# Optimization experiments

Hardware: AMD Instinct MI355X
Metric: run time of the kernel (lower is better)

Reference implementation:

```python
import jax, jax.numpy as jnp
import numpy as np


def setup_inputs() -> dict:
    key = jax.random.key(0)
    k1, k2, k3, k4 = jax.random.split(key, 4)
    B, S, D = 8, 2048, 512
    scale = 1.0 / np.sqrt(D)
    return {
        "x": jax.random.normal(k1, (B, S, D), dtype=jnp.float32),
        "WQ": jax.random.normal(k2, (D, D), dtype=jnp.float32) * scale,
        "WK": jax.random.normal(k3, (D, D), dtype=jnp.float32) * scale,
        "WV": jax.random.normal(k4, (D, D), dtype=jnp.float32) * scale,
    }


def reference(x, WQ, WK, WV):
    # x: [B, S, D]; single-head scaled dot-product self-attention
    Q = jnp.einsum("bsd,de->bse", x, WQ)
    K = jnp.einsum("bsd,de->bse", x, WK)
    V = jnp.einsum("bsd,de->bse", x, WV)
    d_k = jnp.asarray(K.shape[-1], dtype=x.dtype)
    scores = jnp.einsum("bqd,bkd->bqk", Q, K) / jnp.sqrt(d_k)  # [B,S,S]
    weights = jax.nn.softmax(scores, axis=-1)
    return jnp.einsum("bqk,bkd->bqd", weights, V)
```

## Files before the change

### kernel.cpp

```cpp
#include <hip/hip_runtime.h>
#include <cstdint>
#include <cstddef>

#define B_ 8
#define S_ 2048
#define D_ 512

typedef float f32x4 __attribute__((ext_vector_type(4)));
typedef __bf16 bf16x8 __attribute__((ext_vector_type(8)));

__device__ __forceinline__ unsigned short f2bf(float f) {
    unsigned u = __builtin_bit_cast(unsigned, f);
    u += 0x7FFFu + ((u >> 16) & 1u);
    return (unsigned short)(u >> 16);
}

__device__ __forceinline__ void gll16(const void* g, void* l) {
    __builtin_amdgcn_global_load_lds(
        (const __attribute__((address_space(1))) unsigned int*)g,
        (__attribute__((address_space(3))) unsigned int*)l, 16, 0, 0);
}

#define VMCNT(n) asm volatile("s_waitcnt vmcnt(%0)" :: "i"(n) : "memory")
#define LGKM0()  asm volatile("s_waitcnt lgkmcnt(0)" ::: "memory")
#define SBAR()   __builtin_amdgcn_s_barrier()
#define SCHED0() __builtin_amdgcn_sched_barrier(0)

template<int AMT, int BNT>
__global__ __launch_bounds__(512, 2) void gemm8(
    const unsigned short* __restrict__ A,
    const unsigned short* __restrict__ B,
    void* __restrict__ Cv,
    unsigned short* __restrict__ Cv2,
    int K, int lda, int ldb, int ldc, int ntn)
{
    constexpr int BM     = 64 * AMT;
    constexpr int BN     = 128 * BNT;
    constexpr int ABYTES = BM * 128;
    constexpr int BBYTES = BN * 128;
    constexpr int AH     = ABYTES / 2;
    constexpr int BH     = BBYTES / 2;
    constexpr int AGL    = AMT / 2;
    constexpr int BGL    = BNT;
    constexpr int BUFB   = ABYTES + BBYTES;
    __shared__ __align__(16) char lds[2 * BUFB];

    const int tq  = blockIdx.x;
    const int tn  = tq % ntn;
    const int tm  = tq / ntn;
    const int m0   = tm * BM;
    const int n0   = tn * BN;
    const int tid  = threadIdx.x;
    const int lane = tid & 63;
    const int w    = tid >> 6;
    const int g2   = w >> 2;
    const int nb   = w & 3;

    const int lrow = lane >> 3;
    const int swz  = ((lane & 7) ^ lrow) << 3;
    const unsigned short* gA[2][AGL];
    const unsigned short* gB[2][BGL];
    #pragma unroll
    for (int h = 0; h < 2; ++h) {
        #pragma unroll
        for (int i = 0; i < AGL; ++i)
            gA[h][i] = A + (size_t)(m0 + h * (BM / 2) + (w * AGL + i) * 8 + lrow) * lda + swz;
        #pragma unroll
        for (int i = 0; i < BGL; ++i)
            gB[h][i] = B + (size_t)(n0 + h * (BN / 2) + (w * BGL + i) * 8 + lrow) * ldb + swz;
    }
    auto stA = [&](int bs, int h, int kof) {
        #pragma unroll
        for (int i = 0; i < AGL; ++i)
            gll16(gA[h][i] + kof, lds + bs * BUFB + h * AH + (w * AGL + i) * 1024);
    };
    auto stB = [&](int bs, int h, int kof) {
        #pragma unroll
        for (int i = 0; i < BGL; ++i)
            gll16(gB[h][i] + kof, lds + bs * BUFB + ABYTES + h * BH + (w * BGL + i) * 1024);
    };

    const int fr = lane & 15;
    const int gq = lane >> 4;
    const int c0 = (gq ^ (fr & 7)) << 4;
    int aoff[AMT], boff[BNT];
    #pragma unroll
    for (int ml = 0; ml < AMT; ++ml)
        aoff[ml] = (g2 * (16 * AMT) + ml * 16 + fr) * 128 + c0;
    #pragma unroll
    for (int nl = 0; nl < BNT; ++nl)
        boff[nl] = (nb * (16 * BNT) + nl * 16 + fr) * 128 + c0;

    bf16x8 af[2 * AMT], bLO[2 * BNT], bHI[2 * BNT];
    f32x4 acc[2 * AMT][2 * BNT] = {};

    auto ldA = [&](const char* Ab, int mh) {
        #pragma unroll
        for (int ml = 0; ml < AMT; ++ml)
            #pragma unroll
            for (int kk = 0; kk < 2; ++kk)
                af[ml * 2 + kk] = *(const bf16x8*)(Ab + mh * AH + (aoff[ml] ^ (kk << 6)));
    };
    auto ldB = [&](const char* Bb, int nh, bf16x8* bf) {
        #pragma unroll
        for (int nl = 0; nl < BNT; ++nl)
            #pragma unroll
            for (int kk = 0; kk < 2; ++kk)
                bf[nl * 2 + kk] = *(const bf16x8*)(Bb + nh * BH + (boff[nl] ^ (kk << 6)));
    };
    auto mma = [&](int mh, int nh, const bf16x8* bf) {
        __builtin_amdgcn_s_setprio(1);
        #pragma unroll
        for (int ml = 0; ml < AMT; ++ml)
            #pragma unroll
            for (int nl = 0; nl < BNT; ++nl)
                #pragma unroll
                for (int kk = 0; kk < 2; ++kk)
                    acc[mh * AMT + ml][nh * BNT + nl] =
                        __builtin_amdgcn_mfma_f32_16x16x32_bf16(
                            af[ml * 2 + kk], bf[nl * 2 + kk],
                            acc[mh * AMT + ml][nh * BNT + nl], 0, 0, 0);
        __builtin_amdgcn_s_setprio(0);
    };

    stA(0, 0, 0);  stB(0, 0, 0);
    stA(0, 1, 0);  stB(0, 1, 0);
    stA(1, 0, 64); stB(1, 0, 64);

    const int NT = K >> 6;
    for (int tt = 0; tt < NT; ++tt) {
        const int bs = tt & 1;
        const char* Ab = lds + bs * BUFB;
        const char* Bb = Ab + ABYTES;
        const bool last = (tt == NT - 1);

        if (!last) stA(bs ^ 1, 1, (tt + 1) << 6);
        if (last) { VMCNT(AGL + BGL); } else { VMCNT(6); }
        SBAR(); SCHED0();
        ldA(Ab, 0); ldB(Bb, 0, bLO);
        mma(0, 0, bLO);

        if (!last) stB(bs ^ 1, 1, (tt + 1) << 6);
        if (last) { VMCNT(0); } else { VMCNT(6); }
        SBAR(); SCHED0();
        ldB(Bb, 1, bHI);
        mma(0, 1, bHI);

        if (tt + 2 < NT) stA(bs, 0, (tt + 2) << 6);
        VMCNT(6);
        SBAR(); SCHED0();
        ldA(Ab, 1);
        mma(1, 0, bLO);

        if (tt + 2 < NT) stB(bs, 0, (tt + 2) << 6);
        VMCNT(6);
        SBAR(); SCHED0();
        mma(1, 1, bHI);
    }

    const int rb4 = gq << 2;
#define AB_(mt) ((((mt) / AMT) * (BM / 2)) + g2 * (16 * AMT) + ((mt) % AMT) * 16)
#define BB_(nt) ((((nt) / BNT) * (BN / 2)) + nb * (16 * BNT) + ((nt) % BNT) * 16)
    if (tn >= 4) {
        #pragma unroll
        for (int mt = 0; mt < 2 * AMT; ++mt) {
            const int s0q = m0 + AB_(mt) + rb4;
            const int b   = s0q >> 11;
            const int se  = s0q & (S_ - 1);
            #pragma unroll
            for (int nt = 0; nt < 2 * BNT; ++nt) {
                const int d = (n0 - 2 * D_) + BB_(nt) + fr;
                ushort4 u;
                u.x = f2bf(acc[mt][nt][0]);
                u.y = f2bf(acc[mt][nt][1]);
                u.z = f2bf(acc[mt][nt][2]);
                u.w = f2bf(acc[mt][nt][3]);
                *(ushort4*)&Cv2[((size_t)b * D_ + d) * S_ + se] = u;
            }
        }
    } else {
        unsigned short* C = (unsigned short*)Cv;
        #pragma unroll
        for (int mt = 0; mt < 2 * AMT; ++mt)
            #pragma unroll
            for (int nt = 0; nt < 2 * BNT; ++nt) {
                const int gc = n0 + BB_(nt) + fr;
                #pragma unroll
                for (int r = 0; r < 4; ++r)
                    C[(size_t)(m0 + AB_(mt) + rb4 + r) * ldc + gc] = f2bf(acc[mt][nt][r]);
            }
    }
#undef AB_
#undef BB_
}

__global__ __launch_bounds__(512, 2) void fused_attn(
    const unsigned short* __restrict__ qk,
    const unsigned short* __restrict__ vtb,
    float* __restrict__ out,
    float scale)
{
    __shared__ __align__(16) char lds[148480];
    char* const RING = lds;
    char* const PB   = lds + 131072;
    float* const RS  = (float*)(lds + 147456);

    const int lin = blockIdx.x;
    const int bz  = lin & 7;
    const int q0  = (lin >> 3) * 64;
    const int tid = threadIdx.x;
    const int lane = tid & 63;
    const int w   = tid >> 6;
    const int fr  = lane & 15;
    const int gq  = lane >> 4;
    const int g2  = w >> 2;
    const int nb  = w & 3;
    const int k7  = fr & 7;

    int row4[4], sc4[4];
    #pragma unroll
    for (int i = 0; i < 4; ++i) {
        const int off = tid * 16 + i * 8192;
        row4[i] = off >> 8;
        sc4[i]  = ((((off >> 4) & 15) ^ (row4[i] & 7)) << 3);
    }
    const size_t qrowb = (size_t)bz * S_;

    auto stK = [&](int slot, int kv0, int j) {
        #pragma unroll
        for (int i = 0; i < 4; ++i)
            gll16(qk + (qrowb + kv0 + row4[i]) * 1024 + 512 + j * 128 + sc4[i],
                  RING + slot * 32768 + tid * 16 + i * 8192);
    };
    auto stV = [&](int slot, int kv0, int c) {
        #pragma unroll
        for (int i = 0; i < 4; ++i)
            gll16(vtb + ((size_t)bz * D_ + c * 128 + row4[i]) * S_ + kv0 + sc4[i],
                  RING + slot * 32768 + tid * 16 + i * 8192);
    };

    bf16x8 qreg[16];
    #pragma unroll
    for (int c = 0; c < 16; ++c)
        qreg[c] = *(const bf16x8*)(
            qk + (qrowb + q0 + nb * 16 + fr) * 1024 + c * 32 + gq * 8);
    SCHED0();

    f32x4 acc_pv[4][4] = {};
    float rsl = 0.f;

    stK(0, 0, 0); stK(1, 0, 1);
    SCHED0();

    for (int kvi = 0; kvi < 16; ++kvi) {
        const int kv0 = kvi * 128;
        f32x4 acc_s[4] = {};

        #pragma unroll
        for (int j = 0; j < 4; ++j) {
            if (j < 2) { VMCNT(4); } else { VMCNT(8); }
            SBAR(); SCHED0();
            if      (j == 0) stK(2, kv0, 2);
            else if (j == 1) { stK(3, kv0, 3); stV(0, kv0, 0); }
            else if (j == 2) stV(1, kv0, 1);
            else             stV(2, kv0, 2);
            SCHED0();
            const char* Kb = RING + j * 32768;
            __builtin_amdgcn_s_setprio(1);
            #pragma unroll
            for (int kk = 0; kk < 4; ++kk) {
                const int ch = ((kk * 4 + gq) ^ k7) << 4;
                #pragma unroll
                for (int mt = 0; mt < 4; ++mt) {
                    const bf16x8 kf = *(const bf16x8*)(
                        Kb + (g2 * 64 + mt * 16 + fr) * 256 + ch);
                    acc_s[mt] = __builtin_amdgcn_mfma_f32_16x16x32_bf16(
                        kf, qreg[j * 4 + kk], acc_s[mt], 0, 0, 0);
                }
            }
            __builtin_amdgcn_s_setprio(0);
        }

        #pragma unroll
        for (int mt = 0; mt < 4; ++mt) {
            float p0 = __expf(acc_s[mt][0] * scale);
            float p1 = __expf(acc_s[mt][1] * scale);
            float p2 = __expf(acc_s[mt][2] * scale);
            float p3 = __expf(acc_s[mt][3] * scale);
            rsl += (p0 + p1) + (p2 + p3);
            ushort4 u;
            u.x = f2bf(p0); u.y = f2bf(p1); u.z = f2bf(p2); u.w = f2bf(p3);
            const int row   = nb * 16 + fr;
            const int chunk = g2 * 8 + mt * 2 + (gq >> 1);
            *(ushort4*)(PB + row * 256 + ((chunk ^ k7) << 4) + (gq & 1) * 8) = u;
        }
        LGKM0();
        VMCNT(4);
        SBAR(); SCHED0();
        stV(3, kv0, 3);
        SCHED0();
        __builtin_amdgcn_s_setprio(1);
        #pragma unroll
        for (int ks = 0; ks < 4; ++ks) {
            const int ch = ((ks * 4 + gq) ^ k7) << 4;
            const bf16x8 vf0 = *(const bf16x8*)(RING + (w * 16 + fr) * 256 + ch);
            const bf16x8 vf1 = *(const bf16x8*)(RING + 32768 + (w * 16 + fr) * 256 + ch);
            #pragma unroll
            for (int nt2 = 0; nt2 < 4; ++nt2) {
                const bf16x8 pf = *(const bf16x8*)(PB + (nt2 * 16 + fr) * 256 + ch);
                acc_pv[0][nt2] = __builtin_amdgcn_mfma_f32_16x16x32_bf16(
                    vf0, pf, acc_pv[0][nt2], 0, 0, 0);
                acc_pv[1][nt2] = __builtin_amdgcn_mfma_f32_16x16x32_bf16(
                    vf1, pf, acc_pv[1][nt2], 0, 0, 0);
            }
        }
        __builtin_amdgcn_s_setprio(0);

        VMCNT(0);
        SBAR(); SCHED0();
        if (kvi < 15) { stK(0, kv0 + 128, 0); stK(1, kv0 + 128, 1); }
        SCHED0();
        __builtin_amdgcn_s_setprio(1);
        #pragma unroll
        for (int ks = 0; ks < 4; ++ks) {
            const int ch = ((ks * 4 + gq) ^ k7) << 4;
            const bf16x8 vf2 = *(const bf16x8*)(RING + 65536 + (w * 16 + fr) * 256 + ch);
            const bf16x8 vf3 = *(const bf16x8*)(RING + 98304 + (w * 16 + fr) * 256 + ch);
            #pragma unroll
            for (int nt2 = 0; nt2 < 4; ++nt2) {
                const bf16x8 pf = *(const bf16x8*)(PB + (nt2 * 16 + fr) * 256 + ch);
                acc_pv[2][nt2] = __builtin_amdgcn_mfma_f32_16x16x32_bf16(
                    vf2, pf, acc_pv[2][nt2], 0, 0, 0);
                acc_pv[3][nt2] = __builtin_amdgcn_mfma_f32_16x16x32_bf16(
                    vf3, pf, acc_pv[3][nt2], 0, 0, 0);
            }
        }
        __builtin_amdgcn_s_setprio(0);
    }

    rsl += __shfl_xor(rsl, 16);
    rsl += __shfl_xor(rsl, 32);
    if (lane < 16) RS[g2 * 64 + nb * 16 + lane] = rsl;
    __syncthreads();

    #pragma unroll
    for (int nt2 = 0; nt2 < 4; ++nt2) {
        const int q = nt2 * 16 + fr;
        const float inv = __builtin_amdgcn_rcpf(RS[q] + RS[64 + q]);
        float* op = out + ((qrowb + q0 + q) * D_);
        #pragma unroll
        for (int c = 0; c < 4; ++c) {
            const int d0 = c * 128 + w * 16 + gq * 4;
            float4 o;
            o.x = acc_pv[c][nt2][0] * inv;
            o.y = acc_pv[c][nt2][1] * inv;
            o.z = acc_pv[c][nt2][2] * inv;
            o.w = acc_pv[c][nt2][3] * inv;
            *(float4*)(op + d0) = o;
        }
    }
}

__global__ __launch_bounds__(256) void convert_x4(const float* __restrict__ x,
                                                  unsigned short* __restrict__ xb) {
    const size_t i = ((size_t)blockIdx.x * 256 + threadIdx.x) * 4;
    const float4 f = *(const float4*)(x + i);
    ushort4 u;
    u.x = f2bf(f.x); u.y = f2bf(f.y); u.z = f2bf(f.z); u.w = f2bf(f.w);
    *(ushort4*)(xb + i) = u;
}

__global__ __launch_bounds__(256) void convert_w(const float* __restrict__ WQ,
                                                 const float* __restrict__ WK,
                                                 const float* __restrict__ WV,
                                                 unsigned short* __restrict__ WT) {
    const int o = blockIdx.x * 256 + threadIdx.x;
    const float* W = blockIdx.y == 0 ? WQ : (blockIdx.y == 1 ? WK : WV);
    const int e = o >> 9, d = o & (D_ - 1);
    WT[(size_t)blockIdx.y * D_ * D_ + o] = f2bf(W[d * D_ + e]);
}

extern "C" void kernel_launch(void* const* d_in, const int* in_sizes, int n_in,
                              void* d_out, int out_size, void* d_ws, size_t ws_size,
                              hipStream_t stream)
{
    const float* x  = (const float*)d_in[0];
    const float* WQ = (const float*)d_in[1];
    const float* WK = (const float*)d_in[2];
    const float* WV = (const float*)d_in[3];

    unsigned short* ws  = (unsigned short*)d_ws;
    const size_t NX = (size_t)B_ * S_ * D_;
    unsigned short* xb  = ws;
    unsigned short* wtb = xb + NX;
    unsigned short* qk  = wtb + 3 * D_ * D_;
    unsigned short* vtb = qk + NX * 2;

    convert_x4<<<dim3((unsigned)(NX / 4 / 256)), 256, 0, stream>>>(x, xb);
    convert_w<<<dim3(D_ * D_ / 256, 3), 256, 0, stream>>>(WQ, WK, WV, wtb);

    gemm8<4, 2><<<dim3(384), 512, 0, stream>>>(
        xb, wtb, qk, vtb, D_, D_, D_, 2 * D_,  6);

    fused_attn<<<dim3(256), 512, 0, stream>>>(
        qk, vtb, (float*)d_out, 0.04419417382415922f);
}
```

Before: 225.6 us.

## Switch fused attention MFMAs from 16x16x32 to 32x32x16 tiles

Replaces the 16x16x32 bf16 MFMA tiling with 32x32x16 instructions for both QK^T and PV. Waves are reassigned so each computes a 32-kv by 32-query score tile, and PV tiles cover 32 output dims by 64 queries. The larger tiles cut LDS fragment loads per FLOP and the number of MFMA issues. In exchange, Q registers double (32 bf16x8 fragments), which raises register pressure at 2 blocks per CU, and the row-sum reduction now spans four wave groups.

```diff
diff --git a/kernel.cpp b/kernel.cpp
--- a/kernel.cpp
+++ b/kernel.cpp
@@ -7,6 +7,7 @@
 #define D_ 512
 
 typedef float f32x4 __attribute__((ext_vector_type(4)));
+typedef float f32x16 __attribute__((ext_vector_type(16)));
 typedef __bf16 bf16x8 __attribute__((ext_vector_type(8)));
 
 __device__ __forceinline__ unsigned short f2bf(float f) {
@@ -210,12 +211,12 @@
     const int q0  = (lin >> 3) * 64;
     const int tid = threadIdx.x;
     const int lane = tid & 63;
-    const int w   = tid >> 6;
-    const int fr  = lane & 15;
-    const int gq  = lane >> 4;
-    const int g2  = w >> 2;
-    const int nb  = w & 3;
-    const int k7  = fr & 7;
+    const int w    = tid >> 6;
+    const int fr32 = lane & 31;
+    const int hi   = lane >> 5;
+    const int g4   = w >> 1;
+    const int qh   = w & 1;
+    const int k7x  = fr32 & 7;
 
     int row4[4], sc4[4];
     #pragma unroll
@@ -239,14 +240,14 @@
                   RING + slot * 32768 + tid * 16 + i * 8192);
     };
 
-    bf16x8 qreg[16];
+    bf16x8 qreg[32];
     #pragma unroll
-    for (int c = 0; c < 16; ++c)
+    for (int c = 0; c < 32; ++c)
         qreg[c] = *(const bf16x8*)(
-            qk + (qrowb + q0 + nb * 16 + fr) * 1024 + c * 32 + gq * 8);
+            qk + (qrowb + q0 + qh * 32 + fr32) * 1024 + c * 16 + hi * 8);
     SCHED0();
 
-    f32x4 acc_pv[4][4] = {};
+    f32x16 accA0 = {}, accA1 = {}, accB0 = {}, accB1 = {};
     float rsl = 0.f;
 
     stK(0, 0, 0); stK(1, 0, 1);
@@ -254,7 +255,7 @@
 
     for (int kvi = 0; kvi < 16; ++kvi) {
         const int kv0 = kvi * 128;
-        f32x4 acc_s[4] = {};
+        f32x16 acc_s = {};
 
         #pragma unroll
         for (int j = 0; j < 4; ++j) {
@@ -268,97 +269,97 @@
             const char* Kb = RING + j * 32768;
             __builtin_amdgcn_s_setprio(1);
             #pragma unroll
-            for (int kk = 0; kk < 4; ++kk) {
-                const int ch = ((kk * 4 + gq) ^ k7) << 4;
-                #pragma unroll
-                for (int mt = 0; mt < 4; ++mt) {
-                    const bf16x8 kf = *(const bf16x8*)(
-                        Kb + (g2 * 64 + mt * 16 + fr) * 256 + ch);
-                    acc_s[mt] = __builtin_amdgcn_mfma_f32_16x16x32_bf16(
-                        kf, qreg[j * 4 + kk], acc_s[mt], 0, 0, 0);
-                }
+            for (int c = 0; c < 8; ++c) {
+                const int ch = (((c << 1) | hi) ^ k7x) << 4;
+                const bf16x8 kf = *(const bf16x8*)(
+                    Kb + (g4 * 32 + fr32) * 256 + ch);
+                acc_s = __builtin_amdgcn_mfma_f32_32x32x16_bf16(
+                    kf, qreg[j * 8 + c], acc_s, 0, 0, 0);
             }
             __builtin_amdgcn_s_setprio(0);
         }
 
         #pragma unroll
-        for (int mt = 0; mt < 4; ++mt) {
-            float p0 = __expf(acc_s[mt][0] * scale);
-            float p1 = __expf(acc_s[mt][1] * scale);
-            float p2 = __expf(acc_s[mt][2] * scale);
-            float p3 = __expf(acc_s[mt][3] * scale);
+        for (int k = 0; k < 4; ++k) {
+            float p0 = __expf(acc_s[4 * k + 0] * scale);
+            float p1 = __expf(acc_s[4 * k + 1] * scale);
+            float p2 = __expf(acc_s[4 * k + 2] * scale);
+            float p3 = __expf(acc_s[4 * k + 3] * scale);
             rsl += (p0 + p1) + (p2 + p3);
             ushort4 u;
             u.x = f2bf(p0); u.y = f2bf(p1); u.z = f2bf(p2); u.w = f2bf(p3);
-            const int row   = nb * 16 + fr;
-            const int chunk = g2 * 8 + mt * 2 + (gq >> 1);
-            *(ushort4*)(PB + row * 256 + ((chunk ^ k7) << 4) + (gq & 1) * 8) = u;
+            const int chunk = 4 * g4 + k;
+            *(ushort4*)(PB + (qh * 32 + fr32) * 256 +
+                        ((chunk ^ k7x) << 4) + hi * 8) = u;
         }
         LGKM0();
         VMCNT(4);
         SBAR(); SCHED0();
         stV(3, kv0, 3);
         SCHED0();
-        __builtin_amdgcn_s_setprio(1);
-        #pragma unroll
-        for (int ks = 0; ks < 4; ++ks) {
-            const int ch = ((ks * 4 + gq) ^ k7) << 4;
-            const bf16x8 vf0 = *(const bf16x8*)(RING + (w * 16 + fr) * 256 + ch);
-            const bf16x8 vf1 = *(const bf16x8*)(RING + 32768 + (w * 16 + fr) * 256 + ch);
-            #pragma unroll
-            for (int nt2 = 0; nt2 < 4; ++nt2) {
-                const bf16x8 pf = *(const bf16x8*)(PB + (nt2 * 16 + fr) * 256 + ch);
-                acc_pv[0][nt2] = __builtin_amdgcn_mfma_f32_16x16x32_bf16(
-                    vf0, pf, acc_pv[0][nt2], 0, 0, 0);
-                acc_pv[1][nt2] = __builtin_amdgcn_mfma_f32_16x16x32_bf16(
-                    vf1, pf, acc_pv[1][nt2], 0, 0, 0);
+        {
+            const char* Va = RING + (w >> 2) * 32768;
+            const int vrow = ((w & 3) * 32 + fr32) * 256;
+            __builtin_amdgcn_s_setprio(1);
+            #pragma unroll
+            for (int ks = 0; ks < 8; ++ks) {
+                const int ch = (((ks << 1) | hi) ^ k7x) << 4;
+                const bf16x8 vf  = *(const bf16x8*)(Va + vrow + ch);
+                const bf16x8 pf0 = *(const bf16x8*)(PB + fr32 * 256 + ch);
+                const bf16x8 pf1 = *(const bf16x8*)(PB + (32 + fr32) * 256 + ch);
+                accA0 = __builtin_amdgcn_mfma_f32_32x32x16_bf16(vf, pf0, accA0, 0, 0, 0);
+                accA1 = __builtin_amdgcn_mfma_f32_32x32x16_bf16(vf, pf1, accA1, 0, 0, 0);
             }
+            __builtin_amdgcn_s_setprio(0);
         }
-        __builtin_amdgcn_s_setprio(0);
 
         VMCNT(0);
         SBAR(); SCHED0();
         if (kvi < 15) { stK(0, kv0 + 128, 0); stK(1, kv0 + 128, 1); }
         SCHED0();
-        __builtin_amdgcn_s_setprio(1);
-        #pragma unroll
-        for (int ks = 0; ks < 4; ++ks) {
-            const int ch = ((ks * 4 + gq) ^ k7) << 4;
-            const bf16x8 vf2 = *(const bf16x8*)(RING + 65536 + (w * 16 + fr) * 256 + ch);
-            const bf16x8 vf3 = *(const bf16x8*)(RING + 98304 + (w * 16 + fr) * 256 + ch);
-            #pragma unroll
-            for (int nt2 = 0; nt2 < 4; ++nt2) {
-                const bf16x8 pf = *(const bf16x8*)(PB + (nt2 * 16 + fr) * 256 + ch);
-                acc_pv[2][nt2] = __builtin_amdgcn_mfma_f32_16x16x32_bf16(
-                    vf2, pf, acc_pv[2][nt2], 0, 0, 0);
-                acc_pv[3][nt2] = __builtin_amdgcn_mfma_f32_16x16x32_bf16(
-                    vf3, pf, acc_pv[3][nt2], 0, 0, 0);
+        {
+            const char* Vb = RING + (2 + (w >> 2)) * 32768;
+            const int vrow = ((w & 3) * 32 + fr32) * 256;
+            __builtin_amdgcn_s_setprio(1);
+            #pragma unroll
+            for (int ks = 0; ks < 8; ++ks) {
+                const int ch = (((ks << 1) | hi) ^ k7x) << 4;
+                const bf16x8 vf  = *(const bf16x8*)(Vb + vrow + ch);
+                const bf16x8 pf0 = *(const bf16x8*)(PB + fr32 * 256 + ch);
+                const bf16x8 pf1 = *(const bf16x8*)(PB + (32 + fr32) * 256 + ch);
+                accB0 = __builtin_amdgcn_mfma_f32_32x32x16_bf16(vf, pf0, accB0, 0, 0, 0);
+                accB1 = __builtin_amdgcn_mfma_f32_32x32x16_bf16(vf, pf1, accB1, 0, 0, 0);
             }
+            __builtin_amdgcn_s_setprio(0);
         }
-        __builtin_amdgcn_s_setprio(0);
-    }
-
-    rsl += __shfl_xor(rsl, 16);
+    }
+
     rsl += __shfl_xor(rsl, 32);
-    if (lane < 16) RS[g2 * 64 + nb * 16 + lane] = rsl;
+    if (lane < 32) RS[g4 * 64 + qh * 32 + fr32] = rsl;
     __syncthreads();
 
-    #pragma unroll
-    for (int nt2 = 0; nt2 < 4; ++nt2) {
-        const int q = nt2 * 16 + fr;
-        const float inv = __builtin_amdgcn_rcpf(RS[q] + RS[64 + q]);
-        float* op = out + ((qrowb + q0 + q) * D_);
-        #pragma unroll
-        for (int c = 0; c < 4; ++c) {
-            const int d0 = c * 128 + w * 16 + gq * 4;
-            float4 o;
-            o.x = acc_pv[c][nt2][0] * inv;
-            o.y = acc_pv[c][nt2][1] * inv;
-            o.z = acc_pv[c][nt2][2] * inv;
-            o.w = acc_pv[c][nt2][3] * inv;
-            *(float4*)(op + d0) = o;
-        }
-    }
+#define STORE_TILE(ACC, DBASE, QB)                                          \
+    {                                                                       \
+        const int q = (QB) * 32 + fr32;                                     \
+        const float inv = __builtin_amdgcn_rcpf(                            \
+            (RS[q] + RS[64 + q]) + (RS[128 + q] + RS[192 + q]));            \
+        float* op = out + ((qrowb + q0 + q) * D_);                          \
+        _Pragma("unroll")                                                   \
+        for (int k = 0; k < 4; ++k) {                                       \
+            const int d0 = (DBASE) * 32 + 8 * k + 4 * hi;                   \
+            float4 o;                                                       \
+            o.x = (ACC)[4 * k + 0] * inv;                                   \
+            o.y = (ACC)[4 * k + 1] * inv;                                   \
+            o.z = (ACC)[4 * k + 2] * inv;                                   \
+            o.w = (ACC)[4 * k + 3] * inv;                                   \
+            *(float4*)(op + d0) = o;                                        \
+        }                                                                   \
+    }
+    STORE_TILE(accA0, w,     0)
+    STORE_TILE(accA1, w,     1)
+    STORE_TILE(accB0, w + 8, 0)
+    STORE_TILE(accB1, w + 8, 1)
+#undef STORE_TILE
 }
 
 __global__ __launch_bounds__(256) void convert_x4(const float* __restrict__ x,
```

After: 267.9 us. 1.19x slower.
